# Kernel optimization log

Hardware: AMD Instinct MI355X
Metric: run time of the kernel (lower is better)

## Reference

```python
import jax, jax.numpy as jnp
import numpy as np

VOCAB, EMB, UNITS, B, T = 32000, 256, 1024, 64, 128


def setup_inputs() -> dict:
    key = jax.random.key(0)
    ks = jax.random.split(key, 16)
    s = lambda fan_in: 1.0 / np.sqrt(fan_in)
    inp = {
        "x": jax.random.randint(ks[0], (B, 1), 0, VOCAB),
        "hidden": jax.random.normal(ks[1], (B, UNITS), dtype=jnp.float32),
        "enc_output": jax.random.normal(ks[2], (B, T, UNITS), dtype=jnp.float32),
        "emb": jax.random.normal(ks[3], (VOCAB, EMB), dtype=jnp.float32) * 0.02,
        "W1": jax.random.normal(ks[4], (UNITS, UNITS), dtype=jnp.float32) * s(UNITS),
        "b1": jnp.zeros((UNITS,), jnp.float32),
        "W2": jax.random.normal(ks[5], (UNITS, UNITS), dtype=jnp.float32) * s(UNITS),
        "b2": jnp.zeros((UNITS,), jnp.float32),
        "V": jax.random.normal(ks[6], (UNITS, 1), dtype=jnp.float32) * s(UNITS),
        "bV": jnp.zeros((1,), jnp.float32),
        "gru_k": jax.random.normal(ks[7], (UNITS + EMB, 3 * UNITS), dtype=jnp.float32) * s(UNITS + EMB),
        "gru_rk": jax.random.normal(ks[8], (UNITS, 3 * UNITS), dtype=jnp.float32) * s(UNITS),
        "gru_b": jnp.zeros((3 * UNITS,), jnp.float32),
        "fc_W": jax.random.normal(ks[9], (UNITS, VOCAB), dtype=jnp.float32) * s(UNITS),
        "fc_b": jnp.zeros((VOCAB,), jnp.float32),
    }
    return inp


def reference(x, hidden, enc_output, emb, W1, b1, W2, b2, V, bV,
              gru_k, gru_rk, gru_b, fc_W, fc_b):
    # Bahdanau additive attention over encoder steps
    # score: [B, T, 1]
    score = jnp.tanh(enc_output @ W1 + b1 + (hidden @ W2 + b2)[:, None, :]) @ V + bV
    attention_weights = jax.nn.softmax(score, axis=1)              # [B, T, 1]
    context = jnp.sum(attention_weights * enc_output, axis=1)      # [B, UNITS]

    xe = emb[x[:, 0]]                                              # [B, EMB]
    gin = jnp.concatenate([context, xe], axis=-1)                  # [B, UNITS+EMB]

    # Single GRU step; original calls gru(x) with no initial_state -> h0 = 0
    h0 = jnp.zeros((x.shape[0], gru_rk.shape[0]), gin.dtype)
    u = x.shape[1]  # unused; seq len is 1
    gates_x = gin @ gru_k + gru_b                                  # [B, 3*UNITS]
    gates_h = h0 @ gru_rk                                          # [B, 3*UNITS]
    n = gru_rk.shape[0]
    z = jax.nn.sigmoid(gates_x[:, :n] + gates_h[:, :n])
    r = jax.nn.sigmoid(gates_x[:, n:2 * n] + gates_h[:, n:2 * n])
    hh = jnp.tanh(gates_x[:, 2 * n:] + r * gates_h[:, 2 * n:])
    state = z * h0 + (1.0 - z) * hh                                # [B, UNITS]

    logits = state @ fc_W + fc_b                                   # [B, VOCAB]
    return logits, state, attention_weights
```

## Files before the change

### kernel.cpp

```cpp
#include <hip/hip_runtime.h>
#include <math.h>

#define UNITS 1024
#define EMBD  256
#define BATCH 64
#define TLEN  128
#define VOCAB 32000
#define GIN_D (UNITS + EMBD)

typedef short short8 __attribute__((ext_vector_type(8)));
typedef float f32x4  __attribute__((ext_vector_type(4)));

__device__ __forceinline__ unsigned short f2bf(float f) {
    unsigned int u = __float_as_uint(f);
    u += 0x7fffu + ((u >> 16) & 1u);
    return (unsigned short)(u >> 16);
}

__global__ __launch_bounds__(256) void k_w1t(const float* __restrict__ W1,
                                             unsigned short* __restrict__ w1t) {
    __shared__ float t[64][65];
    const int tid = threadIdx.x;
    const int bx = blockIdx.x * 64;
    const int by = blockIdx.y * 64;
#pragma unroll
    for (int p = 0; p < 16; ++p) {
        const int idx = tid + p * 256;
        const int r = idx >> 6, cc = idx & 63;
        t[r][cc] = W1[(size_t)(bx + r) * UNITS + by + cc];
    }
    __syncthreads();
#pragma unroll
    for (int p = 0; p < 16; ++p) {
        const int idx = tid + p * 256;
        const int jr = idx >> 6, kc = idx & 63;
        w1t[(size_t)(by + jr) * UNITS + bx + kc] = f2bf(t[kc][jr]);
    }
}

__global__ __launch_bounds__(256) void k_c(const float* __restrict__ hidden,
                                           const float* __restrict__ W2,
                                           const float* __restrict__ b1,
                                           const float* __restrict__ b2,
                                           float* __restrict__ c) {
    const int lane = threadIdx.x & 63;
    const int j = blockIdx.x * 64 + lane;
    const int b = blockIdx.y * 4 + (threadIdx.x >> 6);
    const int k0 = blockIdx.z * 256;
    const float* hrow = hidden + (size_t)b * UNITS + k0;
    const float* wcol = W2 + (size_t)k0 * UNITS + j;
    float acc = 0.f;
#pragma unroll 8
    for (int k = 0; k < 256; ++k)
        acc = fmaf(hrow[k], wcol[(size_t)k * UNITS], acc);
    if (blockIdx.z == 0) acc += b1[j] + b2[j];
    atomicAdd(&c[(size_t)b * UNITS + j], acc);
}

__global__ __launch_bounds__(256, 4) void k_score(const float* __restrict__ enc,
                                                  const unsigned short* __restrict__ w1t,
                                                  const float* __restrict__ c,
                                                  const float* __restrict__ V,
                                                  float* __restrict__ score) {
    __shared__ unsigned short As[64 * 72];
    __shared__ unsigned short Bs[128 * 72];
    const int half = blockIdx.x & 1;
    const int b    = blockIdx.x >> 1;
    const int jt   = blockIdx.y;
    const int tid  = threadIdx.x;
    const int lane = tid & 63;
    const int wc   = tid >> 6;
    const int quad = lane >> 4;
    const int l16  = lane & 15;

    const float* encb = enc + (size_t)b * TLEN * UNITS + (size_t)half * 64 * UNITS;
    const unsigned short* w1b = w1t + (size_t)jt * 128 * UNITS;

    f32x4 acc[4][2];
#pragma unroll
    for (int i = 0; i < 4; ++i)
#pragma unroll
        for (int j = 0; j < 2; ++j)
            acc[i][j] = (f32x4){0.f, 0.f, 0.f, 0.f};

    const int ar = tid >> 4;
    const int ac = tid & 15;

    for (int kc = 0; kc < UNITS; kc += 64) {
        float4 av[4];
#pragma unroll
        for (int rr = 0; rr < 4; ++rr)
            av[rr] = *(const float4*)(encb + (size_t)(ar + rr * 16) * UNITS + kc + ac * 4);
        short8 bv[4];
#pragma unroll
        for (int p = 0; p < 4; ++p) {
            const int cidx = tid + p * 256;
            const int row = cidx >> 3, ch = cidx & 7;
            bv[p] = *(const short8*)(w1b + (size_t)row * UNITS + kc + ch * 8);
        }
        __syncthreads();
#pragma unroll
        for (int rr = 0; rr < 4; ++rr) {
            ushort4 h;
            h.x = f2bf(av[rr].x); h.y = f2bf(av[rr].y);
            h.z = f2bf(av[rr].z); h.w = f2bf(av[rr].w);
            *(ushort4*)&As[(ar + rr * 16) * 72 + ac * 4] = h;
        }
#pragma unroll
        for (int p = 0; p < 4; ++p) {
            const int cidx = tid + p * 256;
            const int row = cidx >> 3, ch = cidx & 7;
            *(short8*)&Bs[row * 72 + ch * 8] = bv[p];
        }
        __syncthreads();
#pragma unroll
        for (int kk = 0; kk < 2; ++kk) {
            const int kb = kk * 32 + quad * 8;
            short8 af[4], bfr[2];
#pragma unroll
            for (int mt = 0; mt < 4; ++mt)
                af[mt] = *(const short8*)&As[(mt * 16 + l16) * 72 + kb];
#pragma unroll
            for (int nt = 0; nt < 2; ++nt)
                bfr[nt] = *(const short8*)&Bs[(wc * 32 + nt * 16 + l16) * 72 + kb];
#pragma unroll
            for (int mt = 0; mt < 4; ++mt)
#pragma unroll
                for (int nt = 0; nt < 2; ++nt)
                    acc[mt][nt] = __builtin_amdgcn_mfma_f32_16x16x32_bf16(
                        af[mt], bfr[nt], acc[mt][nt], 0, 0, 0);
        }
    }

    float cv[2], vv[2];
#pragma unroll
    for (int nt = 0; nt < 2; ++nt) {
        const int col = jt * 128 + wc * 32 + nt * 16 + l16;
        cv[nt] = c[(size_t)b * UNITS + col];
        vv[nt] = V[col];
    }
    float rs[16];
#pragma unroll
    for (int mt = 0; mt < 4; ++mt)
#pragma unroll
        for (int reg = 0; reg < 4; ++reg) {
            float s = 0.f;
#pragma unroll
            for (int nt = 0; nt < 2; ++nt)
                s += tanhf(acc[mt][nt][reg] + cv[nt]) * vv[nt];
            rs[mt * 4 + reg] = s;
        }
#pragma unroll
    for (int off = 1; off < 16; off <<= 1)
#pragma unroll
        for (int i = 0; i < 16; ++i)
            rs[i] += __shfl_xor(rs[i], off);
    if (l16 == 0) {
#pragma unroll
        for (int mt = 0; mt < 4; ++mt)
#pragma unroll
            for (int reg = 0; reg < 4; ++reg)
                atomicAdd(&score[b * TLEN + half * 64 + mt * 16 + quad * 4 + reg],
                          rs[mt * 4 + reg]);
    }
}

__global__ void k_softmax(const float* __restrict__ score, float* __restrict__ attw) {
    const int b = blockIdx.x;
    const int lane = threadIdx.x;
    float s0 = score[b * TLEN + lane];
    float s1 = score[b * TLEN + 64 + lane];
    float m = fmaxf(s0, s1);
#pragma unroll
    for (int off = 1; off < 64; off <<= 1) m = fmaxf(m, __shfl_xor(m, off));
    const float e0 = expf(s0 - m);
    const float e1 = expf(s1 - m);
    float s = e0 + e1;
#pragma unroll
    for (int off = 1; off < 64; off <<= 1) s += __shfl_xor(s, off);
    const float inv = 1.f / s;
    attw[b * TLEN + lane] = e0 * inv;
    attw[b * TLEN + 64 + lane] = e1 * inv;
}

__global__ __launch_bounds__(256) void k_context(const float* __restrict__ enc,
                                                 const float* __restrict__ attw,
                                                 float* __restrict__ gin) {
    const int b = blockIdx.y;
    const int k = blockIdx.x * 256 + threadIdx.x;
    __shared__ float w[TLEN];
    if (threadIdx.x < TLEN) w[threadIdx.x] = attw[b * TLEN + threadIdx.x];
    __syncthreads();
    const float* e = enc + (size_t)b * TLEN * UNITS + k;
    float acc = 0.f;
#pragma unroll 8
    for (int t = 0; t < TLEN; ++t)
        acc = fmaf(w[t], e[(size_t)t * UNITS], acc);
    gin[(size_t)b * GIN_D + k] = acc;
}

__global__ void k_embed(const int* __restrict__ x, const float* __restrict__ emb,
                        float* __restrict__ gin) {
    const int b = blockIdx.x;
    const int e = threadIdx.x;
    const int row = x[b];
    gin[(size_t)b * GIN_D + UNITS + e] = emb[(size_t)row * EMBD + e];
}

__global__ __launch_bounds__(256) void k_gru_acc(const float* __restrict__ gin,
                                                 const float* __restrict__ gru_k,
                                                 const float* __restrict__ gru_b,
                                                 float* __restrict__ gz,
                                                 float* __restrict__ gh) {
    const int lane = threadIdx.x & 63;
    const int i = blockIdx.x * 64 + lane;
    const int b = blockIdx.y * 4 + (threadIdx.x >> 6);
    const int k0 = blockIdx.z * 256;
    const float* g = gin + (size_t)b * GIN_D + k0;
    const float* wz = gru_k + (size_t)k0 * 3072 + i;
    const float* wh = wz + 2048;
    float az = 0.f, ah = 0.f;
#pragma unroll 8
    for (int k = 0; k < 256; ++k) {
        const float gv = g[k];
        az = fmaf(gv, wz[(size_t)k * 3072], az);
        ah = fmaf(gv, wh[(size_t)k * 3072], ah);
    }
    if (blockIdx.z == 0) { az += gru_b[i]; ah += gru_b[2048 + i]; }
    atomicAdd(&gz[(size_t)b * UNITS + i], az);
    atomicAdd(&gh[(size_t)b * UNITS + i], ah);
}

__global__ __launch_bounds__(256) void k_gru_fin(const float* __restrict__ gz,
                                                 const float* __restrict__ gh,
                                                 float* __restrict__ state,
                                                 float* __restrict__ stateT) {
    const int lane = threadIdx.x & 63;
    const int i = blockIdx.x * 64 + lane;
    const int b = blockIdx.y * 4 + (threadIdx.x >> 6);
    const float az = gz[(size_t)b * UNITS + i];
    const float ah = gh[(size_t)b * UNITS + i];
    const float z = 1.f / (1.f + expf(-az));
    const float hh = tanhf(ah);
    const float st = (1.f - z) * hh;
    state[(size_t)b * UNITS + i] = st;
    stateT[(size_t)i * BATCH + b] = st;
}

__global__ __launch_bounds__(256, 2) void k_fc(const float* __restrict__ stateT,
                                               const float* __restrict__ fc_W,
                                               const float* __restrict__ fc_b,
                                               float* __restrict__ logits) {
    __shared__ float sState[1024 * 16];
    const int tid  = threadIdx.x;
    const int lane = tid & 63;
    const int wid  = tid >> 6;
    const int g0   = blockIdx.y * 16;
    const int col0 = blockIdx.x * 256 + lane * 4;

#pragma unroll
    for (int it = 0; it < 16; ++it) {
        const int idx = tid + it * 256;
        const int r = idx >> 2, cch = idx & 3;
        const float4 v = *(const float4*)(stateT + (size_t)r * BATCH + g0 + cch * 4);
        *(float4*)&sState[r * 16 + cch * 4] = v;
    }

    const int krow0 = wid * 256;
    const float* wbase = fc_W + col0;

    float4 wr[4];
#pragma unroll
    for (int j = 0; j < 4; ++j)
        wr[j] = *(const float4*)(wbase + (size_t)(krow0 + j) * VOCAB);

    __syncthreads();

    float4 acc[16];
#pragma unroll
    for (int b = 0; b < 16; ++b) acc[b] = (float4){0.f, 0.f, 0.f, 0.f};

    float4 srng[2][4];
#pragma unroll
    for (int c = 0; c < 4; ++c)
        srng[0][c] = *(const float4*)&sState[krow0 * 16 + c * 4];

#define FC_SUBSTEP(J, PREFETCH_W, PREFETCH_S)                                  \
    {                                                                          \
        const int r = krow0 + k + (J);                                         \
        if (PREFETCH_S) {                                                      \
            _Pragma("unroll")                                                  \
            for (int c = 0; c < 4; ++c)                                        \
                srng[((J) + 1) & 1][c] = *(const float4*)&sState[(r + 1) * 16 + c * 4]; \
        }                                                                      \
        const float4 wv = wr[(J)];                                             \
        if (PREFETCH_W)                                                        \
            wr[(J)] = *(const float4*)(wbase + (size_t)(r + 4) * VOCAB);       \
        _Pragma("unroll")                                                      \
        for (int c = 0; c < 4; ++c) {                                          \
            const float4 sv = srng[(J) & 1][c];                                \
            acc[c * 4 + 0].x = fmaf(wv.x, sv.x, acc[c * 4 + 0].x);             \
            acc[c * 4 + 0].y = fmaf(wv.y, sv.x, acc[c * 4 + 0].y);             \
            acc[c * 4 + 0].z = fmaf(wv.z, sv.x, acc[c * 4 + 0].z);             \
            acc[c * 4 + 0].w = fmaf(wv.w, sv.x, acc[c * 4 + 0].w);             \
            acc[c * 4 + 1].x = fmaf(wv.x, sv.y, acc[c * 4 + 1].x);             \
            acc[c * 4 + 1].y = fmaf(wv.y, sv.y, acc[c * 4 + 1].y);             \
            acc[c * 4 + 1].z = fmaf(wv.z, sv.y, acc[c * 4 + 1].z);             \
            acc[c * 4 + 1].w = fmaf(wv.w, sv.y, acc[c * 4 + 1].w);             \
            acc[c * 4 + 2].x = fmaf(wv.x, sv.z, acc[c * 4 + 2].x);             \
            acc[c * 4 + 2].y = fmaf(wv.y, sv.z, acc[c * 4 + 2].y);             \
            acc[c * 4 + 2].z = fmaf(wv.z, sv.z, acc[c * 4 + 2].z);             \
            acc[c * 4 + 2].w = fmaf(wv.w, sv.z, acc[c * 4 + 2].w);             \
            acc[c * 4 + 3].x = fmaf(wv.x, sv.w, acc[c * 4 + 3].x);             \
            acc[c * 4 + 3].y = fmaf(wv.y, sv.w, acc[c * 4 + 3].y);             \
            acc[c * 4 + 3].z = fmaf(wv.z, sv.w, acc[c * 4 + 3].z);             \
            acc[c * 4 + 3].w = fmaf(wv.w, sv.w, acc[c * 4 + 3].w);             \
        }                                                                      \
    }

    for (int k = 0; k < 252; k += 4) {
        FC_SUBSTEP(0, true, true)
        FC_SUBSTEP(1, true, true)
        FC_SUBSTEP(2, true, true)
        FC_SUBSTEP(3, true, true)
    }
    {
        const int k = 252;
        FC_SUBSTEP(0, false, true)
        FC_SUBSTEP(1, false, true)
        FC_SUBSTEP(2, false, true)
        FC_SUBSTEP(3, false, false)
    }
#undef FC_SUBSTEP

    __syncthreads();
    float* rbuf = sState;
#pragma unroll 1
    for (int ph = 0; ph < 4; ++ph) {
        if (wid == ph) {
#pragma unroll
            for (int b = 0; b < 16; ++b) {
                float4* p = (float4*)&rbuf[b * 256 + lane * 4];
                if (ph == 0) {
                    *p = acc[b];
                } else {
                    float4 t = *p;
                    t.x += acc[b].x; t.y += acc[b].y;
                    t.z += acc[b].z; t.w += acc[b].w;
                    *p = t;
                }
            }
        }
        __syncthreads();
    }

    const int bb = tid >> 4;
    const int ch = tid & 15;
    const int cbase = blockIdx.x * 256 + ch * 16;
    float* lp = logits + (size_t)(g0 + bb) * VOCAB + cbase;
#pragma unroll
    for (int q = 0; q < 4; ++q) {
        float4 t = *(float4*)&rbuf[bb * 256 + ch * 16 + q * 4];
        const float4 fb = *(const float4*)(fc_b + cbase + q * 4);
        t.x += fb.x; t.y += fb.y; t.z += fb.z; t.w += fb.w;
        *(float4*)(lp + q * 4) = t;
    }
}

extern "C" void kernel_launch(void* const* d_in, const int* in_sizes, int n_in,
                              void* d_out, int out_size, void* d_ws, size_t ws_size,
                              hipStream_t stream) {
    const int*   x      = (const int*)  d_in[0];
    const float* hidden = (const float*)d_in[1];
    const float* enc    = (const float*)d_in[2];
    const float* emb    = (const float*)d_in[3];
    const float* W1     = (const float*)d_in[4];
    const float* b1     = (const float*)d_in[5];
    const float* W2     = (const float*)d_in[6];
    const float* b2     = (const float*)d_in[7];
    const float* V      = (const float*)d_in[8];
    const float* gru_k  = (const float*)d_in[10];
    const float* gru_b  = (const float*)d_in[12];
    const float* fc_W   = (const float*)d_in[13];
    const float* fc_b   = (const float*)d_in[14];

    float* out       = (float*)d_out;
    float* logits    = out;
    float* state_out = out + (size_t)BATCH * VOCAB;
    float* attw      = state_out + (size_t)BATCH * UNITS;

    float* c      = (float*)d_ws;
    float* score  = c + 65536;
    float* gin    = score + 8192;
    float* stateT = gin + 81920;
    float* gz     = stateT + 65536;
    float* gh     = gz + 65536;
    unsigned short* w1t = (unsigned short*)(gh + 65536);

    hipMemsetAsync(c, 0, (size_t)BATCH * UNITS * sizeof(float), stream);
    hipMemsetAsync(score, 0, (size_t)BATCH * TLEN * sizeof(float), stream);
    hipMemsetAsync(gz, 0, (size_t)2 * BATCH * UNITS * sizeof(float), stream);

    k_w1t    <<<dim3(16, 16),    256, 0, stream>>>(W1, w1t);
    k_c      <<<dim3(16, 16, 4), 256, 0, stream>>>(hidden, W2, b1, b2, c);
    k_score  <<<dim3(128, 8),    256, 0, stream>>>(enc, w1t, c, V, score);
    k_softmax<<<64, 64, 0, stream>>>(score, attw);
    k_context<<<dim3(4, 64),     256, 0, stream>>>(enc, attw, gin);
    k_embed  <<<64, 256, 0, stream>>>(x, emb, gin);
    k_gru_acc<<<dim3(16, 16, 5), 256, 0, stream>>>(gin, gru_k, gru_b, gz, gh);
    k_gru_fin<<<dim3(16, 16),    256, 0, stream>>>(gz, gh, state_out, stateT);
    k_fc     <<<dim3(125, 4),    256, 0, stream>>>(stateT, fc_W, fc_b, logits);
}
```

Before: 408.9 us.

## Register-block batch rows in GEMV kernels and remap fc blocks across XCDs

k_c and k_gru_acc now stage a 16-row slice of the input vectors in shared memory, and each thread accumulates 4 batch rows per weight load. This cuts weight global loads by 4x and shrinks the grid by 4x. k_fc uses a flattened 512-block grid whose index is remapped so that blocks sharing fc_W columns land on the same XCD, to improve L2 reuse. Padding blocks exit early. The trade-off is fewer blocks in the GEMV kernels (less parallelism) and more registers per thread.

```diff
diff --git a/kernel.cpp b/kernel.cpp
--- a/kernel.cpp
+++ b/kernel.cpp
@@ -43,18 +43,39 @@
                                            const float* __restrict__ b1,
                                            const float* __restrict__ b2,
                                            float* __restrict__ c) {
-    const int lane = threadIdx.x & 63;
-    const int j = blockIdx.x * 64 + lane;
-    const int b = blockIdx.y * 4 + (threadIdx.x >> 6);
+    __shared__ float sH[16][256];
+    const int tid = threadIdx.x;
+    const int j = blockIdx.x * 64 + (tid & 63);
+    const int g = tid >> 6;
+    const int b0 = blockIdx.y * 16;
     const int k0 = blockIdx.z * 256;
-    const float* hrow = hidden + (size_t)b * UNITS + k0;
+#pragma unroll
+    for (int p = 0; p < 4; ++p) {
+        const int fidx = tid + p * 256;
+        const int row = fidx >> 6, c4 = fidx & 63;
+        *(float4*)&sH[row][c4 * 4] =
+            *(const float4*)(hidden + (size_t)(b0 + row) * UNITS + k0 + c4 * 4);
+    }
+    __syncthreads();
     const float* wcol = W2 + (size_t)k0 * UNITS + j;
-    float acc = 0.f;
+    float acc[4] = {0.f, 0.f, 0.f, 0.f};
+    const int bb0 = g * 4;
 #pragma unroll 8
-    for (int k = 0; k < 256; ++k)
-        acc = fmaf(hrow[k], wcol[(size_t)k * UNITS], acc);
-    if (blockIdx.z == 0) acc += b1[j] + b2[j];
-    atomicAdd(&c[(size_t)b * UNITS + j], acc);
+    for (int k = 0; k < 256; ++k) {
+        const float w = wcol[(size_t)k * UNITS];
+        acc[0] = fmaf(w, sH[bb0 + 0][k], acc[0]);
+        acc[1] = fmaf(w, sH[bb0 + 1][k], acc[1]);
+        acc[2] = fmaf(w, sH[bb0 + 2][k], acc[2]);
+        acc[3] = fmaf(w, sH[bb0 + 3][k], acc[3]);
+    }
+    if (blockIdx.z == 0) {
+        const float bias = b1[j] + b2[j];
+#pragma unroll
+        for (int bb = 0; bb < 4; ++bb) acc[bb] += bias;
+    }
+#pragma unroll
+    for (int bb = 0; bb < 4; ++bb)
+        atomicAdd(&c[(size_t)(b0 + bb0 + bb) * UNITS + j], acc[bb]);
 }
 
 __global__ __launch_bounds__(256, 4) void k_score(const float* __restrict__ enc,
@@ -212,23 +233,48 @@
                                                  const float* __restrict__ gru_b,
                                                  float* __restrict__ gz,
                                                  float* __restrict__ gh) {
-    const int lane = threadIdx.x & 63;
-    const int i = blockIdx.x * 64 + lane;
-    const int b = blockIdx.y * 4 + (threadIdx.x >> 6);
+    __shared__ float sG[16][256];
+    const int tid = threadIdx.x;
+    const int i = blockIdx.x * 64 + (tid & 63);
+    const int g = tid >> 6;
+    const int b0 = blockIdx.y * 16;
     const int k0 = blockIdx.z * 256;
-    const float* g = gin + (size_t)b * GIN_D + k0;
+#pragma unroll
+    for (int p = 0; p < 4; ++p) {
+        const int fidx = tid + p * 256;
+        const int row = fidx >> 6, c4 = fidx & 63;
+        *(float4*)&sG[row][c4 * 4] =
+            *(const float4*)(gin + (size_t)(b0 + row) * GIN_D + k0 + c4 * 4);
+    }
+    __syncthreads();
     const float* wz = gru_k + (size_t)k0 * 3072 + i;
     const float* wh = wz + 2048;
-    float az = 0.f, ah = 0.f;
-#pragma unroll 8
+    float az[4] = {0.f, 0.f, 0.f, 0.f};
+    float ah[4] = {0.f, 0.f, 0.f, 0.f};
+    const int bb0 = g * 4;
+#pragma unroll 4
     for (int k = 0; k < 256; ++k) {
-        const float gv = g[k];
-        az = fmaf(gv, wz[(size_t)k * 3072], az);
-        ah = fmaf(gv, wh[(size_t)k * 3072], ah);
-    }
-    if (blockIdx.z == 0) { az += gru_b[i]; ah += gru_b[2048 + i]; }
-    atomicAdd(&gz[(size_t)b * UNITS + i], az);
-    atomicAdd(&gh[(size_t)b * UNITS + i], ah);
+        const float vz = wz[(size_t)k * 3072];
+        const float vh = wh[(size_t)k * 3072];
+        const float g0 = sG[bb0 + 0][k];
+        const float g1 = sG[bb0 + 1][k];
+        const float g2 = sG[bb0 + 2][k];
+        const float g3 = sG[bb0 + 3][k];
+        az[0] = fmaf(vz, g0, az[0]); ah[0] = fmaf(vh, g0, ah[0]);
+        az[1] = fmaf(vz, g1, az[1]); ah[1] = fmaf(vh, g1, ah[1]);
+        az[2] = fmaf(vz, g2, az[2]); ah[2] = fmaf(vh, g2, ah[2]);
+        az[3] = fmaf(vz, g3, az[3]); ah[3] = fmaf(vh, g3, ah[3]);
+    }
+    if (blockIdx.z == 0) {
+        const float bz = gru_b[i], bh = gru_b[2048 + i];
+#pragma unroll
+        for (int bb = 0; bb < 4; ++bb) { az[bb] += bz; ah[bb] += bh; }
+    }
+#pragma unroll
+    for (int bb = 0; bb < 4; ++bb) {
+        atomicAdd(&gz[(size_t)(b0 + bb0 + bb) * UNITS + i], az[bb]);
+        atomicAdd(&gh[(size_t)(b0 + bb0 + bb) * UNITS + i], ah[bb]);
+    }
 }
 
 __global__ __launch_bounds__(256) void k_gru_fin(const float* __restrict__ gz,
@@ -252,11 +298,18 @@
                                                const float* __restrict__ fc_b,
                                                float* __restrict__ logits) {
     __shared__ float sState[1024 * 16];
+    const int flat = blockIdx.x;
+    const int xcd  = flat & 7;
+    const int rest = flat >> 3;
+    const int by   = rest & 3;
+    const int bx   = (rest >> 2) * 8 + xcd;
+    if (bx >= 125) return;
+
     const int tid  = threadIdx.x;
     const int lane = tid & 63;
     const int wid  = tid >> 6;
-    const int g0   = blockIdx.y * 16;
-    const int col0 = blockIdx.x * 256 + lane * 4;
+    const int g0   = by * 16;
+    const int col0 = bx * 256 + lane * 4;
 
 #pragma unroll
     for (int it = 0; it < 16; ++it) {
@@ -356,7 +409,7 @@
 
     const int bb = tid >> 4;
     const int ch = tid & 15;
-    const int cbase = blockIdx.x * 256 + ch * 16;
+    const int cbase = bx * 256 + ch * 16;
     float* lp = logits + (size_t)(g0 + bb) * VOCAB + cbase;
 #pragma unroll
     for (int q = 0; q < 4; ++q) {
@@ -402,12 +455,12 @@
     hipMemsetAsync(gz, 0, (size_t)2 * BATCH * UNITS * sizeof(float), stream);
 
     k_w1t    <<<dim3(16, 16),    256, 0, stream>>>(W1, w1t);
-    k_c      <<<dim3(16, 16, 4), 256, 0, stream>>>(hidden, W2, b1, b2, c);
+    k_c      <<<dim3(16, 4, 4),  256, 0, stream>>>(hidden, W2, b1, b2, c);
     k_score  <<<dim3(128, 8),    256, 0, stream>>>(enc, w1t, c, V, score);
     k_softmax<<<64, 64, 0, stream>>>(score, attw);
     k_context<<<dim3(4, 64),     256, 0, stream>>>(enc, attw, gin);
     k_embed  <<<64, 256, 0, stream>>>(x, emb, gin);
-    k_gru_acc<<<dim3(16, 16, 5), 256, 0, stream>>>(gin, gru_k, gru_b, gz, gh);
+    k_gru_acc<<<dim3(16, 4, 5),  256, 0, stream>>>(gin, gru_k, gru_b, gz, gh);
     k_gru_fin<<<dim3(16, 16),    256, 0, stream>>>(gz, gh, state_out, stateT);
-    k_fc     <<<dim3(125, 4),    256, 0, stream>>>(stateT, fc_W, fc_b, logits);
-}
+    k_fc     <<<dim3(512),       256, 0, stream>>>(stateT, fc_W, fc_b, logits);
+}
```

New measurement: 400.8 us. 1.02x faster.
